# Kernel tuning notes

Hardware: AMD Instinct MI355X
Metric: run time of the kernel (lower is better)

Reference implementation:

```python
import jax, jax.numpy as jnp
import numpy as np

B, C, HC, H, W = 4, 512, 64, 64, 64


def _spectral_norm(Wm, u):
    # one torch-style power iteration; u,v are treated as constants (detached)
    v = Wm.T @ u
    v = v / jnp.maximum(jnp.linalg.norm(v), 1e-12)
    u2 = Wm @ v
    u2 = u2 / jnp.maximum(jnp.linalg.norm(u2), 1e-12)
    u2 = jax.lax.stop_gradient(u2)
    v = jax.lax.stop_gradient(v)
    sigma = u2 @ (Wm @ v)
    return Wm / sigma


def setup_inputs() -> dict:
    key = jax.random.key(0)
    ks = jax.random.split(key, 14)
    return {
        "x": jax.random.normal(ks[0], (B, C, H, W), jnp.float32),
        "Wf": jax.random.normal(ks[1], (HC, C), jnp.float32) * 0.05,
        "bf": jax.random.normal(ks[2], (HC,), jnp.float32) * 0.05,
        "Wg": jax.random.normal(ks[3], (HC, C), jnp.float32) * 0.05,
        "bg": jax.random.normal(ks[4], (HC,), jnp.float32) * 0.05,
        "Wh": jax.random.normal(ks[5], (HC, C), jnp.float32) * 0.05,
        "bh": jax.random.normal(ks[6], (HC,), jnp.float32) * 0.05,
        "Wv": jax.random.normal(ks[7], (C, HC), jnp.float32) * 0.05,
        "bv": jax.random.normal(ks[8], (C,), jnp.float32) * 0.05,
        "uf": jax.random.normal(ks[9], (HC,), jnp.float32),
        "ug": jax.random.normal(ks[10], (HC,), jnp.float32),
        "uh": jax.random.normal(ks[11], (HC,), jnp.float32),
        "uv": jax.random.normal(ks[12], (C,), jnp.float32),
        "gamma": jax.random.normal(ks[13], (1,), jnp.float32),
    }


def reference(x, Wf, bf, Wg, bg, Wh, bh, Wv, bv, uf, ug, uh, uv, gamma):
    nb, nc, imgh, imgw = x.shape
    n = imgh * imgw
    xf = x.reshape(nb, nc, n)  # [B, C, N]
    Wf_sn = _spectral_norm(Wf, uf)
    Wg_sn = _spectral_norm(Wg, ug)
    Wh_sn = _spectral_norm(Wh, uh)
    Wv_sn = _spectral_norm(Wv, uv)
    # 1x1 convs are per-pixel GEMMs
    f = jnp.einsum('kc,bcn->bkn', Wf_sn, xf) + bf[:, None]  # [B, HC, N]
    g = jnp.einsum('kc,bcn->bkn', Wg_sn, xf) + bg[:, None]
    h = jnp.einsum('kc,bcn->bkn', Wh_sn, xf) + bh[:, None]
    s = jnp.einsum('bkn,bkm->bnm', f, g)       # [B, N, N] scores
    beta = jax.nn.softmax(s, axis=-1)
    o = jnp.einsum('bnm,bkm->bkn', beta, h)    # [B, HC, N] (already transposed)
    out = jnp.einsum('ck,bkn->bcn', Wv_sn, o) + bv[:, None]
    out = out.reshape(nb, nc, imgh, imgw)
    return gamma[0] * out + x
```

## Files before the change

kernel.cpp:

```cpp
#include <hip/hip_runtime.h>
#include <hip/hip_bf16.h>

typedef __attribute__((ext_vector_type(8))) short short8;
typedef __attribute__((ext_vector_type(4))) float floatx4;
typedef __attribute__((ext_vector_type(16))) float floatx16;
typedef unsigned short ushortt;

#define LOG2E 1.4426950408889634f

__device__ __forceinline__ float fast_exp2(float x) {
    return __builtin_amdgcn_exp2f(x);
}
__device__ __forceinline__ ushortt f2bf(float f) {
    unsigned int u = __float_as_uint(f);
    u += 0x7fffu + ((u >> 16) & 1u);
    return (ushortt)(u >> 16);
}
__device__ __forceinline__ unsigned int f2bf_pk(float a, float b) {
    float2 t; t.x = a; t.y = b;
    __hip_bfloat162 h = __float22bfloat162_rn(t);
    return *reinterpret_cast<unsigned int*>(&h);
}
__device__ __forceinline__ float bf2f(ushortt h) {
    return __uint_as_float(((unsigned int)h) << 16);
}

__device__ __forceinline__ float block_sum(float v, float* red) {
    #pragma unroll
    for (int off = 32; off > 0; off >>= 1) v += __shfl_down(v, off);
    int wid = threadIdx.x >> 6, ln = threadIdx.x & 63;
    __syncthreads();
    if (ln == 0) red[wid] = v;
    __syncthreads();
    return red[0] + red[1] + red[2] + red[3];
}

__global__ __launch_bounds__(256) void sigma_kernel(
    const float* __restrict__ Wf, const float* __restrict__ uf,
    const float* __restrict__ Wg, const float* __restrict__ ug,
    const float* __restrict__ Wh, const float* __restrict__ uh,
    const float* __restrict__ Wv, const float* __restrict__ uv,
    float* __restrict__ sig) {
    __shared__ float tv[512];
    __shared__ float tvp[256];
    __shared__ float zpart[256];
    __shared__ float red[4];
    const int mat = blockIdx.x, tid = threadIdx.x;

    if (mat < 3) {
        const float* W = (mat == 0) ? Wf : ((mat == 1) ? Wg : Wh);
        const float* u = (mat == 0) ? uf : ((mat == 1) ? ug : uh);
        for (int c = tid; c < 512; c += 256) {
            float s0 = 0.f;
            #pragma unroll 8
            for (int r = 0; r < 64; ++r) s0 += W[r * 512 + c] * u[r];
            tv[c] = s0;
        }
        __syncthreads();
        float p = tv[tid] * tv[tid] + tv[tid + 256] * tv[tid + 256];
        float nt2 = block_sum(p, red);
        float nt = fmaxf(sqrtf(nt2), 1e-12f);
        {
            int r = tid & 63, qq = tid >> 6;
            const float* Wr = W + r * 512 + qq * 128;
            const float* tq = tv + qq * 128;
            float part = 0.f;
            #pragma unroll 16
            for (int c = 0; c < 128; ++c) part += Wr[c] * tq[c];
            zpart[tid] = part;
        }
        __syncthreads();
        if (tid < 64) {
            float z = zpart[tid] + zpart[tid + 64] + zpart[tid + 128] + zpart[tid + 192];
            z = z * z;
            #pragma unroll
            for (int off = 32; off > 0; off >>= 1) z += __shfl_xor(z, off);
            if (tid == 0) sig[mat] = sqrtf(z) / nt;
        }
    } else {
        const float* W = Wv; const float* u = uv;
        {
            int c = tid & 63, rs = tid >> 6;
            float s0 = 0.f;
            #pragma unroll 8
            for (int r = rs * 128; r < rs * 128 + 128; ++r) s0 += W[r * 64 + c] * u[r];
            tvp[tid] = s0;
        }
        __syncthreads();
        if (tid < 64) tv[tid] = tvp[tid] + tvp[tid + 64] + tvp[tid + 128] + tvp[tid + 192];
        __syncthreads();
        float t = (tid < 64) ? tv[tid] : 0.f;
        float nt2 = block_sum(t * t, red);
        float nt = fmaxf(sqrtf(nt2), 1e-12f);
        {
            const float* w1 = W + (size_t)tid * 64;
            const float* w2 = W + (size_t)(tid + 256) * 64;
            float z1 = 0.f, z2 = 0.f;
            #pragma unroll 8
            for (int c = 0; c < 64; ++c) {
                float tc = tv[c];
                z1 += w1[c] * tc;
                z2 += w2[c] * tc;
            }
            float zp = z1 * z1 + z2 * z2;
            float z2t = block_sum(zp, red);
            if (tid == 0) sig[3] = sqrtf(z2t) / nt;
        }
    }
}

__global__ __launch_bounds__(256) void prep_w_kernel(
    const float* __restrict__ Wf, const float* __restrict__ Wg,
    const float* __restrict__ Wh, const float* __restrict__ Wv,
    const float* __restrict__ sig,
    ushortt* __restrict__ wqkv, ushortt* __restrict__ wvb) {
    int idx = blockIdx.x * 256 + threadIdx.x;
    if (idx < 98304) {
        int k = idx >> 9, c = idx & 511;
        int which = k >> 6;
        const float* W = (which == 0) ? Wf : ((which == 1) ? Wg : Wh);
        float inv = 1.0f / sig[which];
        wqkv[idx] = f2bf(W[(k & 63) * 512 + c] * inv);
    } else {
        int o = idx - 98304;
        wvb[o] = f2bf(Wv[o] / sig[3]);
    }
}

__global__ __launch_bounds__(256, 4) void qkv_kernel(
    const float* __restrict__ x, const ushortt* __restrict__ wqkv,
    const float* __restrict__ bfv, const float* __restrict__ bgv,
    const float* __restrict__ bhv,
    ushortt* __restrict__ Qb, ushortt* __restrict__ Kb, ushortt* __restrict__ Vt) {
    __shared__ unsigned int xs[1120];
    const int tid = threadIdx.x;
    const int n0 = blockIdx.x * 32, b = blockIdx.y;
    const int lane = tid & 63, w = tid >> 6;
    const int strip = w & 1, ksel = w >> 1;
    const int q = lane >> 4, l15 = lane & 15;
    const int sn = tid & 31, sg = tid >> 5;

    floatx4 acc[6];
    #pragma unroll
    for (int kt = 0; kt < 6; ++kt) acc[kt] = (floatx4){0.f, 0.f, 0.f, 0.f};

    const float* xb = x + ((size_t)b * 512) * 4096 + n0 + sn;
    float2 pre[4];
    #pragma unroll
    for (int i = 0; i < 4; ++i) {
        int c = sg * 8 + 2 * i;
        pre[i].x = xb[(size_t)c * 4096];
        pre[i].y = xb[(size_t)(c + 1) * 4096];
    }

    for (int c0 = 0; c0 < 512; c0 += 64) {
        __syncthreads();
        {
            uint4 pk;
            pk.x = f2bf_pk(pre[0].x, pre[0].y);
            pk.y = f2bf_pk(pre[1].x, pre[1].y);
            pk.z = f2bf_pk(pre[2].x, pre[2].y);
            pk.w = f2bf_pk(pre[3].x, pre[3].y);
            *reinterpret_cast<uint4*>(&xs[sn * 32 + ((sg ^ (sn & 7)) << 2)]) = pk;
        }
        if (c0 + 64 < 512) {
            #pragma unroll
            for (int i = 0; i < 4; ++i) {
                int c = c0 + 64 + sg * 8 + 2 * i;
                pre[i].x = xb[(size_t)c * 4096];
                pre[i].y = xb[(size_t)(c + 1) * 4096];
            }
        }
        __syncthreads();
        const unsigned int* xr = &xs[(16 * strip + l15) * 32];
        #pragma unroll
        for (int kc = 0; kc < 2; ++kc) {
            union { uint4 v; short8 s8; } af;
            af.v = *reinterpret_cast<const uint4*>(&xr[((4 * kc + q) ^ (l15 & 7)) << 2]);
            #pragma unroll
            for (int kt = 0; kt < 6; ++kt) {
                short8 bb = *reinterpret_cast<const short8*>(
                    &wqkv[(size_t)(ksel * 96 + kt * 16 + l15) * 512 + c0 + kc * 32 + q * 8]);
                acc[kt] = __builtin_amdgcn_mfma_f32_16x16x32_bf16(af.s8, bb, acc[kt], 0, 0, 0);
            }
        }
    }

    const int nloc = n0 + 16 * strip + 4 * q;
    if (ksel == 0) {
        #pragma unroll
        for (int kt = 0; kt < 4; ++kt) {
            int k = kt * 16 + l15;
            float bb = bfv[k];
            #pragma unroll
            for (int r = 0; r < 4; ++r)
                Qb[((size_t)b * 4096 + nloc + r) * 64 + k] = f2bf((acc[kt][r] + bb) * LOG2E);
        }
        #pragma unroll
        for (int kt = 4; kt < 6; ++kt) {
            int k = (kt - 4) * 16 + l15;
            float bb = bgv[k];
            #pragma unroll
            for (int r = 0; r < 4; ++r)
                Kb[((size_t)b * 4096 + nloc + r) * 64 + k] = f2bf(acc[kt][r] + bb);
        }
    } else {
        #pragma unroll
        for (int kt = 0; kt < 2; ++kt) {
            int k = 32 + kt * 16 + l15;
            float bb = bgv[k];
            #pragma unroll
            for (int r = 0; r < 4; ++r)
                Kb[((size_t)b * 4096 + nloc + r) * 64 + k] = f2bf(acc[kt][r] + bb);
        }
    }
    __syncthreads();
    if (ksel == 1) {
        #pragma unroll
        for (int kt = 2; kt < 6; ++kt) {
            int d = (kt - 2) * 16 + l15;
            float bb = bhv[d];
            int base = d * 17 + 8 * strip + 2 * q;
            xs[base]     = f2bf_pk(acc[kt][0] + bb, acc[kt][1] + bb);
            xs[base + 1] = f2bf_pk(acc[kt][2] + bb, acc[kt][3] + bb);
        }
    }
    __syncthreads();
    {
        int d = tid >> 2, sgg = tid & 3;
        uint4 vv;
        vv.x = xs[d * 17 + sgg * 4 + 0]; vv.y = xs[d * 17 + sgg * 4 + 1];
        vv.z = xs[d * 17 + sgg * 4 + 2]; vv.w = xs[d * 17 + sgg * 4 + 3];
        *reinterpret_cast<uint4*>(&Vt[((size_t)b * 64 + d) * 4096 + n0 + sgg * 8]) = vv;
    }
}

__global__ __launch_bounds__(256, 3) void attn_kernel(
    const ushortt* __restrict__ Qb, const ushortt* __restrict__ Kb,
    const ushortt* __restrict__ Vt, ushortt* __restrict__ Opart,
    float2* __restrict__ ml, ushortt* __restrict__ Ob, int KB) {
    __shared__ unsigned int smem[4420];
    const int tid = threadIdx.x;
    const int n0 = blockIdx.x * 64, b = blockIdx.y, s = blockIdx.z;
    const int lane = tid & 63, w = tid >> 6;
    const int qh = w & 1, kh = w >> 1;
    const int l31 = lane & 31, h = lane >> 5;

    const ushortt* Kg = Kb + (size_t)b * 4096 * 64;
    const ushortt* Vg = Vt + (size_t)b * 64 * 4096;

    short8 bq[4];
    {
        const ushortt* Qg = Qb + ((size_t)b * 4096 + n0 + 32 * qh + l31) * 64;
        #pragma unroll
        for (int kc = 0; kc < 4; ++kc)
            bq[kc] = *reinterpret_cast<const short8*>(Qg + kc * 16 + 8 * h);
    }

    floatx16 ot0 = {}, ot1 = {};
    float m_i = -1e30f, l_i = 0.f;

    const int row = tid >> 2, seg = tid & 3;
    const int kbeg = s * KB, kend = kbeg + KB;

    uint4 ck0, ck1, cv0, cv1;
    {
        int nb = kbeg * 64;
        const ushortt* kp = Kg + (size_t)(nb + row) * 64 + seg * 16;
        ck0 = *reinterpret_cast<const uint4*>(kp);
        ck1 = *reinterpret_cast<const uint4*>(kp + 8);
        const ushortt* vp = Vg + (size_t)row * 4096 + nb + seg * 16;
        cv0 = *reinterpret_cast<const uint4*>(vp);
        cv1 = *reinterpret_cast<const uint4*>(vp + 8);
    }

    const int rsw = row & 7;
    for (int kb = kbeg; kb < kend; ++kb) {
        __syncthreads();
        {
            *reinterpret_cast<uint4*>(&smem[row * 32 + (((2 * seg) ^ rsw) << 2)]) = ck0;
            *reinterpret_cast<uint4*>(&smem[row * 32 + (((2 * seg + 1) ^ rsw) << 2)]) = ck1;
            *reinterpret_cast<uint4*>(&smem[2048 + row * 32 + (((2 * seg) ^ rsw) << 2)]) = cv0;
            *reinterpret_cast<uint4*>(&smem[2048 + row * 32 + (((2 * seg + 1) ^ rsw) << 2)]) = cv1;
        }
        if (kb + 1 < kend) {
            int nb = (kb + 1) * 64;
            const ushortt* kp = Kg + (size_t)(nb + row) * 64 + seg * 16;
            ck0 = *reinterpret_cast<const uint4*>(kp);
            ck1 = *reinterpret_cast<const uint4*>(kp + 8);
            const ushortt* vp = Vg + (size_t)row * 4096 + nb + seg * 16;
            cv0 = *reinterpret_cast<const uint4*>(vp);
            cv1 = *reinterpret_cast<const uint4*>(vp + 8);
        }
        __syncthreads();

        floatx16 st = {};
        const unsigned int* kr = &smem[(32 * kh + l31) * 32];
        const int esw = l31 & 7;
        #pragma unroll
        for (int kc = 0; kc < 4; ++kc) {
            union { uint4 v; short8 s8; } af;
            af.v = *reinterpret_cast<const uint4*>(&kr[((2 * kc + h) ^ esw) << 2]);
            st = __builtin_amdgcn_mfma_f32_32x32x16_bf16(af.s8, bq[kc], st, 0, 0, 0);
        }

        float mx = st[0];
        #pragma unroll
        for (int r = 1; r < 16; ++r) mx = fmaxf(mx, st[r]);
        mx = fmaxf(mx, __shfl_xor(mx, 32));
        if (__any(mx > m_i)) {
            float mn = fmaxf(m_i, mx);
            float alpha = fast_exp2(m_i - mn);
            m_i = mn;
            l_i *= alpha;
            #pragma unroll
            for (int r = 0; r < 16; ++r) { ot0[r] *= alpha; ot1[r] *= alpha; }
        }
        float p[16], rs = 0.f;
        #pragma unroll
        for (int r = 0; r < 16; ++r) { p[r] = fast_exp2(st[r] - m_i); rs += p[r]; }
        rs += __shfl_xor(rs, 32);
        l_i += rs;

        unsigned int pk[8], sp[8];
        #pragma unroll
        for (int i = 0; i < 8; ++i) pk[i] = f2bf_pk(p[2 * i], p[2 * i + 1]);
        #pragma unroll
        for (int i = 0; i < 8; ++i) sp[i] = (unsigned int)__shfl_xor((int)pk[i], 32);
        union { unsigned int u[4]; short8 s8; } pb0, pb1;
        pb0.u[0] = h ? sp[2] : pk[0]; pb0.u[1] = h ? sp[3] : pk[1];
        pb0.u[2] = h ? pk[2] : sp[0]; pb0.u[3] = h ? pk[3] : sp[1];
        pb1.u[0] = h ? sp[6] : pk[4]; pb1.u[1] = h ? sp[7] : pk[5];
        pb1.u[2] = h ? pk[6] : sp[4]; pb1.u[3] = h ? pk[7] : sp[5];

        const unsigned int* vr0 = &smem[2048 + l31 * 32];
        const unsigned int* vr1 = &smem[2048 + (32 + l31) * 32];
        #pragma unroll
        for (int c = 0; c < 2; ++c) {
            union { uint4 v; short8 s8; } af;
            af.v = *reinterpret_cast<const uint4*>(&vr0[((4 * kh + 2 * c + h) ^ esw) << 2]);
            ot0 = __builtin_amdgcn_mfma_f32_32x32x16_bf16(af.s8, c ? pb1.s8 : pb0.s8, ot0, 0, 0, 0);
            af.v = *reinterpret_cast<const uint4*>(&vr1[((4 * kh + 2 * c + h) ^ esw) << 2]);
            ot1 = __builtin_amdgcn_mfma_f32_32x32x16_bf16(af.s8, c ? pb1.s8 : pb0.s8, ot1, 0, 0, 0);
        }
    }

    __syncthreads();
    if (h == 0) {
        smem[4160 + w * 32 + l31] = __float_as_uint(m_i);
        smem[4288 + w * 32 + l31] = __float_as_uint(l_i);
    }
    __syncthreads();
    int pw = 2 * (1 - kh) + qh;
    float m2 = __uint_as_float(smem[4160 + pw * 32 + l31]);
    float l2 = __uint_as_float(smem[4288 + pw * 32 + l31]);
    float mstar = fmaxf(m_i, m2);
    float wself = fast_exp2(m_i - mstar);
    float w2 = fast_exp2(m2 - mstar);
    float lm = wself * l_i + w2 * l2;
    float sc = (gridDim.z == 1) ? (wself / lm) : wself;
    if (gridDim.z > 1 && kh == 0 && h == 0) {
        float2 v; v.x = mstar; v.y = lm;
        ml[((size_t)s * 4 + b) * 4096 + n0 + 32 * qh + l31] = v;
    }
    float* om = reinterpret_cast<float*>(smem);
    if (kh == 0) {
        #pragma unroll
        for (int r = 0; r < 16; ++r) {
            int d0 = (r & 3) + 8 * (r >> 2) + 4 * h;
            om[(32 * qh + l31) * 65 + d0] = sc * ot0[r];
            om[(32 * qh + l31) * 65 + 32 + d0] = sc * ot1[r];
        }
    }
    __syncthreads();
    if (kh == 1) {
        #pragma unroll
        for (int r = 0; r < 16; ++r) {
            int d0 = (r & 3) + 8 * (r >> 2) + 4 * h;
            om[(32 * qh + l31) * 65 + d0] += sc * ot0[r];
            om[(32 * qh + l31) * 65 + 32 + d0] += sc * ot1[r];
        }
    }
    __syncthreads();
    {
        int qq = tid >> 2, dsg = tid & 3;
        unsigned int pkk[8];
        #pragma unroll
        for (int j = 0; j < 8; ++j)
            pkk[j] = f2bf_pk(om[qq * 65 + dsg * 16 + 2 * j], om[qq * 65 + dsg * 16 + 2 * j + 1]);
        ushortt* base = (gridDim.z == 1)
            ? (Ob + ((size_t)b * 4096 + n0) * 64)
            : (Opart + (((size_t)s * 4 + b) * 4096 + n0) * 64);
        uint4* d4 = reinterpret_cast<uint4*>(base + (size_t)qq * 64 + dsg * 16);
        uint4 o0; o0.x = pkk[0]; o0.y = pkk[1]; o0.z = pkk[2]; o0.w = pkk[3];
        uint4 o1; o1.x = pkk[4]; o1.y = pkk[5]; o1.z = pkk[6]; o1.w = pkk[7];
        d4[0] = o0; d4[1] = o1;
    }
}

__global__ __launch_bounds__(256) void combine_kernel(
    const ushortt* __restrict__ Opart, const float2* __restrict__ ml,
    ushortt* __restrict__ Ob, int S) {
    const int tid = threadIdx.x;
    const int n0 = blockIdx.x * 64, b = blockIdx.y;
    const int row = n0 + (tid >> 2), dseg = tid & 3;
    float2 mls[4];
    float m = -1e30f;
    for (int s = 0; s < S; ++s) {
        mls[s] = ml[((size_t)s * 4 + b) * 4096 + row];
        m = fmaxf(m, mls[s].x);
    }
    float wgt[4], denom = 0.f;
    for (int s = 0; s < S; ++s) {
        wgt[s] = fast_exp2(mls[s].x - m);
        denom += wgt[s] * mls[s].y;
    }
    float inv = 1.0f / denom;
    float acc[16];
    #pragma unroll
    for (int j = 0; j < 16; ++j) acc[j] = 0.f;
    for (int s = 0; s < S; ++s) {
        const uint4* op = reinterpret_cast<const uint4*>(
            Opart + (((size_t)s * 4 + b) * 4096 + row) * 64 + dseg * 16);
        union { uint4 v; ushortt hh[8]; } u0, u1;
        u0.v = op[0]; u1.v = op[1];
        float ww = wgt[s];
        #pragma unroll
        for (int j = 0; j < 8; ++j) {
            acc[j] += ww * bf2f(u0.hh[j]);
            acc[8 + j] += ww * bf2f(u1.hh[j]);
        }
    }
    union { uint4 u[2]; unsigned int ww[8]; } pkv;
    #pragma unroll
    for (int j = 0; j < 8; ++j) pkv.ww[j] = f2bf_pk(acc[2 * j] * inv, acc[2 * j + 1] * inv);
    uint4* dst = reinterpret_cast<uint4*>(Ob + ((size_t)b * 4096 + row) * 64 + dseg * 16);
    dst[0] = pkv.u[0]; dst[1] = pkv.u[1];
}

__global__ __launch_bounds__(256) void proj_kernel(
    const ushortt* __restrict__ Ob, const ushortt* __restrict__ wvb,
    const float* __restrict__ bv, const float* __restrict__ gamma,
    const float* __restrict__ x, float* __restrict__ out) {
    const int tid = threadIdx.x;
    const int n0 = blockIdx.y * 64, c0 = blockIdx.x * 64, b = blockIdx.z;
    const int w = tid >> 6, lane = tid & 63, q = lane >> 4, l15 = lane & 15;

    short8 a0 = *reinterpret_cast<const short8*>(&wvb[(size_t)(c0 + 16 * w + l15) * 64 + q * 8]);
    short8 a1 = *reinterpret_cast<const short8*>(&wvb[(size_t)(c0 + 16 * w + l15) * 64 + 32 + q * 8]);
    floatx4 acc[4];
    #pragma unroll
    for (int t = 0; t < 4; ++t) acc[t] = (floatx4){0.f, 0.f, 0.f, 0.f};
    #pragma unroll
    for (int t = 0; t < 4; ++t) {
        const ushortt* ob = Ob + ((size_t)b * 4096 + n0 + 16 * t + l15) * 64;
        short8 b0 = *reinterpret_cast<const short8*>(ob + q * 8);
        short8 b1 = *reinterpret_cast<const short8*>(ob + 32 + q * 8);
        acc[t] = __builtin_amdgcn_mfma_f32_16x16x32_bf16(a0, b0, acc[t], 0, 0, 0);
        acc[t] = __builtin_amdgcn_mfma_f32_16x16x32_bf16(a1, b1, acc[t], 0, 0, 0);
    }
    float gm = gamma[0];
    #pragma unroll
    for (int t = 0; t < 4; ++t) {
        #pragma unroll
        for (int r = 0; r < 4; ++r) {
            int c = c0 + 16 * w + 4 * q + r;
            int n = n0 + 16 * t + l15;
            size_t idx = ((size_t)(b * 512 + c)) * 4096 + n;
            out[idx] = gm * (acc[t][r] + bv[c]) + x[idx];
        }
    }
}

extern "C" void kernel_launch(void* const* d_in, const int* in_sizes, int n_in,
                              void* d_out, int out_size, void* d_ws, size_t ws_size,
                              hipStream_t stream) {
    const float* x   = (const float*)d_in[0];
    const float* Wf  = (const float*)d_in[1];
    const float* bf_ = (const float*)d_in[2];
    const float* Wg  = (const float*)d_in[3];
    const float* bg_ = (const float*)d_in[4];
    const float* Wh  = (const float*)d_in[5];
    const float* bh_ = (const float*)d_in[6];
    const float* Wv  = (const float*)d_in[7];
    const float* bv_ = (const float*)d_in[8];
    const float* uf  = (const float*)d_in[9];
    const float* ug  = (const float*)d_in[10];
    const float* uh  = (const float*)d_in[11];
    const float* uv  = (const float*)d_in[12];
    const float* gm  = (const float*)d_in[13];
    float* out = (float*)d_out;

    char* ws = (char*)d_ws;
    float*   sig   = (float*)ws;
    ushortt* wqkv  = (ushortt*)(ws + 256);
    ushortt* wvb   = (ushortt*)(ws + 196864);
    ushortt* Qb    = (ushortt*)(ws + 262400);
    ushortt* Kb    = (ushortt*)(ws + 2359552);
    ushortt* Vt    = (ushortt*)(ws + 4456704);
    ushortt* Ob    = (ushortt*)(ws + 6553856);
    float2*  ml    = (float2*)(ws + 8651008);
    ushortt* Opart = (ushortt*)(ws + 9175296);

    int S = (ws_size >= (size_t)17563904) ? 4 : 1;

    sigma_kernel<<<4, 256, 0, stream>>>(Wf, uf, Wg, ug, Wh, uh, Wv, uv, sig);
    prep_w_kernel<<<512, 256, 0, stream>>>(Wf, Wg, Wh, Wv, sig, wqkv, wvb);
    qkv_kernel<<<dim3(128, 4), 256, 0, stream>>>(x, wqkv, bf_, bg_, bh_, Qb, Kb, Vt);
    attn_kernel<<<dim3(64, 4, S), 256, 0, stream>>>(Qb, Kb, Vt, Opart, ml, Ob, 64 / S);
    if (S > 1) combine_kernel<<<dim3(64, 4), 256, 0, stream>>>(Opart, ml, Ob, S);
    proj_kernel<<<dim3(8, 64, 4), 256, 0, stream>>>(Ob, wvb, bv_, gm, x, out);
}
```

Baseline: 206.9 us.

## Process two key blocks per attention iteration and fuse weight prep into sigma

The attention loop now loads 128 keys/values per iteration into a larger LDS tile and runs two score MFMA chains and one softmax update per pair of blocks. This halves barriers and online-softmax rescales, at the cost of dropping the register prefetch double-buffering. Shared memory per block roughly doubles, which may lower occupancy. Separately, the bf16 weight conversion is folded into the sigma kernel, removing one launch, though only 4 blocks now do the conversion serially.

```diff
diff --git a/kernel.cpp b/kernel.cpp
--- a/kernel.cpp
+++ b/kernel.cpp
@@ -40,11 +40,12 @@
     const float* __restrict__ Wg, const float* __restrict__ ug,
     const float* __restrict__ Wh, const float* __restrict__ uh,
     const float* __restrict__ Wv, const float* __restrict__ uv,
-    float* __restrict__ sig) {
+    float* __restrict__ sig, ushortt* __restrict__ wqkv, ushortt* __restrict__ wvb) {
     __shared__ float tv[512];
     __shared__ float tvp[256];
     __shared__ float zpart[256];
     __shared__ float red[4];
+    __shared__ float sbc;
     const int mat = blockIdx.x, tid = threadIdx.x;
 
     if (mat < 3) {
@@ -75,8 +76,16 @@
             z = z * z;
             #pragma unroll
             for (int off = 32; off > 0; off >>= 1) z += __shfl_xor(z, off);
-            if (tid == 0) sig[mat] = sqrtf(z) / nt;
-        }
+            if (tid == 0) {
+                float sv = sqrtf(z) / nt;
+                sig[mat] = sv;
+                sbc = sv;
+            }
+        }
+        __syncthreads();
+        float inv = 1.0f / sbc;
+        for (int idx = tid; idx < 32768; idx += 256)
+            wqkv[mat * 32768 + idx] = f2bf(W[idx] * inv);
     } else {
         const float* W = Wv; const float* u = uv;
         {
@@ -104,26 +113,11 @@
             }
             float zp = z1 * z1 + z2 * z2;
             float z2t = block_sum(zp, red);
+            float inv = 1.0f / (sqrtf(z2t) / nt);
             if (tid == 0) sig[3] = sqrtf(z2t) / nt;
-        }
-    }
-}
-
-__global__ __launch_bounds__(256) void prep_w_kernel(
-    const float* __restrict__ Wf, const float* __restrict__ Wg,
-    const float* __restrict__ Wh, const float* __restrict__ Wv,
-    const float* __restrict__ sig,
-    ushortt* __restrict__ wqkv, ushortt* __restrict__ wvb) {
-    int idx = blockIdx.x * 256 + threadIdx.x;
-    if (idx < 98304) {
-        int k = idx >> 9, c = idx & 511;
-        int which = k >> 6;
-        const float* W = (which == 0) ? Wf : ((which == 1) ? Wg : Wh);
-        float inv = 1.0f / sig[which];
-        wqkv[idx] = f2bf(W[(k & 63) * 512 + c] * inv);
-    } else {
-        int o = idx - 98304;
-        wvb[o] = f2bf(Wv[o] / sig[3]);
+            for (int idx = tid; idx < 32768; idx += 256)
+                wvb[idx] = f2bf(W[idx] * inv);
+        }
     }
 }
 
@@ -239,7 +233,7 @@
     const ushortt* __restrict__ Qb, const ushortt* __restrict__ Kb,
     const ushortt* __restrict__ Vt, ushortt* __restrict__ Opart,
     float2* __restrict__ ml, ushortt* __restrict__ Ob, int KB) {
-    __shared__ unsigned int smem[4420];
+    __shared__ unsigned int smem[8192];
     const int tid = threadIdx.x;
     const int n0 = blockIdx.x * 64, b = blockIdx.y, s = blockIdx.z;
     const int lane = tid & 63, w = tid >> 6;
@@ -260,53 +254,51 @@
     floatx16 ot0 = {}, ot1 = {};
     float m_i = -1e30f, l_i = 0.f;
 
-    const int row = tid >> 2, seg = tid & 3;
-    const int kbeg = s * KB, kend = kbeg + KB;
-
-    uint4 ck0, ck1, cv0, cv1;
-    {
-        int nb = kbeg * 64;
-        const ushortt* kp = Kg + (size_t)(nb + row) * 64 + seg * 16;
-        ck0 = *reinterpret_cast<const uint4*>(kp);
-        ck1 = *reinterpret_cast<const uint4*>(kp + 8);
-        const ushortt* vp = Vg + (size_t)row * 4096 + nb + seg * 16;
-        cv0 = *reinterpret_cast<const uint4*>(vp);
-        cv1 = *reinterpret_cast<const uint4*>(vp + 8);
-    }
-
-    const int rsw = row & 7;
-    for (int kb = kbeg; kb < kend; ++kb) {
+    const int krow = tid >> 1, khalf = tid & 1;
+    const int vrow = tid >> 2, vq = tid & 3;
+    const int kbeg = s * KB;
+
+    for (int kp = 0; kp < KB; kp += 2) {
+        const int nb = (kbeg + kp) * 64;
         __syncthreads();
         {
-            *reinterpret_cast<uint4*>(&smem[row * 32 + (((2 * seg) ^ rsw) << 2)]) = ck0;
-            *reinterpret_cast<uint4*>(&smem[row * 32 + (((2 * seg + 1) ^ rsw) << 2)]) = ck1;
-            *reinterpret_cast<uint4*>(&smem[2048 + row * 32 + (((2 * seg) ^ rsw) << 2)]) = cv0;
-            *reinterpret_cast<uint4*>(&smem[2048 + row * 32 + (((2 * seg + 1) ^ rsw) << 2)]) = cv1;
-        }
-        if (kb + 1 < kend) {
-            int nb = (kb + 1) * 64;
-            const ushortt* kp = Kg + (size_t)(nb + row) * 64 + seg * 16;
-            ck0 = *reinterpret_cast<const uint4*>(kp);
-            ck1 = *reinterpret_cast<const uint4*>(kp + 8);
-            const ushortt* vp = Vg + (size_t)row * 4096 + nb + seg * 16;
-            cv0 = *reinterpret_cast<const uint4*>(vp);
-            cv1 = *reinterpret_cast<const uint4*>(vp + 8);
-        }
-        __syncthreads();
-
-        floatx16 st = {};
-        const unsigned int* kr = &smem[(32 * kh + l31) * 32];
-        const int esw = l31 & 7;
-        #pragma unroll
-        for (int kc = 0; kc < 4; ++kc) {
-            union { uint4 v; short8 s8; } af;
-            af.v = *reinterpret_cast<const uint4*>(&kr[((2 * kc + h) ^ esw) << 2]);
-            st = __builtin_amdgcn_mfma_f32_32x32x16_bf16(af.s8, bq[kc], st, 0, 0, 0);
-        }
-
-        float mx = st[0];
-        #pragma unroll
-        for (int r = 1; r < 16; ++r) mx = fmaxf(mx, st[r]);
+            const ushortt* kpg = Kg + (size_t)(nb + krow) * 64 + khalf * 32;
+            #pragma unroll
+            for (int j = 0; j < 4; ++j) {
+                int ch = 4 * khalf + j;
+                uint4 v = *reinterpret_cast<const uint4*>(kpg + j * 8);
+                *reinterpret_cast<uint4*>(&smem[krow * 32 + ((ch ^ (krow & 7)) << 2)]) = v;
+            }
+            const ushortt* vpg = Vg + (size_t)vrow * 4096 + nb + vq * 32;
+            #pragma unroll
+            for (int j = 0; j < 4; ++j) {
+                int ch = 4 * vq + j;
+                uint4 v = *reinterpret_cast<const uint4*>(vpg + j * 8);
+                int sw = (ch & 8) | ((ch & 7) ^ (vrow & 7));
+                *reinterpret_cast<uint4*>(&smem[4096 + vrow * 64 + (sw << 2)]) = v;
+            }
+        }
+        __syncthreads();
+
+        floatx16 st0 = {}, st1 = {};
+        {
+            int r0 = 32 * kh + l31;
+            const unsigned int* kr0 = &smem[r0 * 32];
+            const unsigned int* kr1 = &smem[(64 + r0) * 32];
+            const int esw = r0 & 7;
+            #pragma unroll
+            for (int kc = 0; kc < 4; ++kc) {
+                union { uint4 v; short8 s8; } a0, a1;
+                a0.v = *reinterpret_cast<const uint4*>(&kr0[((2 * kc + h) ^ esw) << 2]);
+                a1.v = *reinterpret_cast<const uint4*>(&kr1[((2 * kc + h) ^ esw) << 2]);
+                st0 = __builtin_amdgcn_mfma_f32_32x32x16_bf16(a0.s8, bq[kc], st0, 0, 0, 0);
+                st1 = __builtin_amdgcn_mfma_f32_32x32x16_bf16(a1.s8, bq[kc], st1, 0, 0, 0);
+            }
+        }
+
+        float mx = fmaxf(st0[0], st1[0]);
+        #pragma unroll
+        for (int r = 1; r < 16; ++r) mx = fmaxf(mx, fmaxf(st0[r], st1[r]));
         mx = fmaxf(mx, __shfl_xor(mx, 32));
         if (__any(mx > m_i)) {
             float mn = fmaxf(m_i, mx);
@@ -316,32 +308,52 @@
             #pragma unroll
             for (int r = 0; r < 16; ++r) { ot0[r] *= alpha; ot1[r] *= alpha; }
         }
-        float p[16], rs = 0.f;
-        #pragma unroll
-        for (int r = 0; r < 16; ++r) { p[r] = fast_exp2(st[r] - m_i); rs += p[r]; }
+        float rs = 0.f;
+        #pragma unroll
+        for (int r = 0; r < 16; ++r) {
+            st0[r] = fast_exp2(st0[r] - m_i); rs += st0[r];
+            st1[r] = fast_exp2(st1[r] - m_i); rs += st1[r];
+        }
         rs += __shfl_xor(rs, 32);
         l_i += rs;
 
-        unsigned int pk[8], sp[8];
-        #pragma unroll
-        for (int i = 0; i < 8; ++i) pk[i] = f2bf_pk(p[2 * i], p[2 * i + 1]);
-        #pragma unroll
-        for (int i = 0; i < 8; ++i) sp[i] = (unsigned int)__shfl_xor((int)pk[i], 32);
-        union { unsigned int u[4]; short8 s8; } pb0, pb1;
-        pb0.u[0] = h ? sp[2] : pk[0]; pb0.u[1] = h ? sp[3] : pk[1];
-        pb0.u[2] = h ? pk[2] : sp[0]; pb0.u[3] = h ? pk[3] : sp[1];
-        pb1.u[0] = h ? sp[6] : pk[4]; pb1.u[1] = h ? sp[7] : pk[5];
-        pb1.u[2] = h ? pk[6] : sp[4]; pb1.u[3] = h ? pk[7] : sp[5];
-
-        const unsigned int* vr0 = &smem[2048 + l31 * 32];
-        const unsigned int* vr1 = &smem[2048 + (32 + l31) * 32];
-        #pragma unroll
-        for (int c = 0; c < 2; ++c) {
-            union { uint4 v; short8 s8; } af;
-            af.v = *reinterpret_cast<const uint4*>(&vr0[((4 * kh + 2 * c + h) ^ esw) << 2]);
-            ot0 = __builtin_amdgcn_mfma_f32_32x32x16_bf16(af.s8, c ? pb1.s8 : pb0.s8, ot0, 0, 0, 0);
-            af.v = *reinterpret_cast<const uint4*>(&vr1[((4 * kh + 2 * c + h) ^ esw) << 2]);
-            ot1 = __builtin_amdgcn_mfma_f32_32x32x16_bf16(af.s8, c ? pb1.s8 : pb0.s8, ot1, 0, 0, 0);
+        unsigned int pka[8], pkb[8], spa[8], spb[8];
+        #pragma unroll
+        for (int i = 0; i < 8; ++i) {
+            pka[i] = f2bf_pk(st0[2 * i], st0[2 * i + 1]);
+            pkb[i] = f2bf_pk(st1[2 * i], st1[2 * i + 1]);
+        }
+        #pragma unroll
+        for (int i = 0; i < 8; ++i) {
+            spa[i] = (unsigned int)__shfl_xor((int)pka[i], 32);
+            spb[i] = (unsigned int)__shfl_xor((int)pkb[i], 32);
+        }
+        union { unsigned int u[4]; short8 s8; } pA0, pA1, pB0, pB1;
+        pA0.u[0] = h ? spa[2] : pka[0]; pA0.u[1] = h ? spa[3] : pka[1];
+        pA0.u[2] = h ? pka[2] : spa[0]; pA0.u[3] = h ? pka[3] : spa[1];
+        pA1.u[0] = h ? spa[6] : pka[4]; pA1.u[1] = h ? spa[7] : pka[5];
+        pA1.u[2] = h ? pka[6] : spa[4]; pA1.u[3] = h ? pka[7] : spa[5];
+        pB0.u[0] = h ? spb[2] : pkb[0]; pB0.u[1] = h ? spb[3] : pkb[1];
+        pB0.u[2] = h ? pkb[2] : spb[0]; pB0.u[3] = h ? pkb[3] : spb[1];
+        pB1.u[0] = h ? spb[6] : pkb[4]; pB1.u[1] = h ? spb[7] : pkb[5];
+        pB1.u[2] = h ? pkb[6] : spb[4]; pB1.u[3] = h ? pkb[7] : spb[5];
+
+        const int esw = l31 & 7;
+        const unsigned int* vb0 = &smem[4096 + l31 * 64];
+        const unsigned int* vb1 = &smem[4096 + (32 + l31) * 64];
+        #pragma unroll
+        for (int t = 0; t < 2; ++t) {
+            #pragma unroll
+            for (int c = 0; c < 2; ++c) {
+                int c16 = 8 * t + 4 * kh + 2 * c + h;
+                int sw = ((c16 & 8) | ((c16 & 7) ^ esw)) << 2;
+                short8 pb = t ? (c ? pB1.s8 : pB0.s8) : (c ? pA1.s8 : pA0.s8);
+                union { uint4 v; short8 s8; } af;
+                af.v = *reinterpret_cast<const uint4*>(&vb0[sw]);
+                ot0 = __builtin_amdgcn_mfma_f32_32x32x16_bf16(af.s8, pb, ot0, 0, 0, 0);
+                af.v = *reinterpret_cast<const uint4*>(&vb1[sw]);
+                ot1 = __builtin_amdgcn_mfma_f32_32x32x16_bf16(af.s8, pb, ot1, 0, 0, 0);
+            }
         }
     }
 
@@ -504,8 +516,7 @@
 
     int S = (ws_size >= (size_t)17563904) ? 4 : 1;
 
-    sigma_kernel<<<4, 256, 0, stream>>>(Wf, uf, Wg, ug, Wh, uh, Wv, uv, sig);
-    prep_w_kernel<<<512, 256, 0, stream>>>(Wf, Wg, Wh, Wv, sig, wqkv, wvb);
+    sigma_kernel<<<4, 256, 0, stream>>>(Wf, uf, Wg, ug, Wh, uh, Wv, uv, sig, wqkv, wvb);
     qkv_kernel<<<dim3(128, 4), 256, 0, stream>>>(x, wqkv, bf_, bg_, bh_, Qb, Kb, Vt);
     attn_kernel<<<dim3(64, 4, S), 256, 0, stream>>>(Qb, Kb, Vt, Opart, ml, Ob, 64 / S);
     if (S > 1) combine_kernel<<<dim3(64, 4), 256, 0, stream>>>(Opart, ml, Ob, S);
```

Result: slower. 228.1 us (+10.2%).
